# Optimization experiments

Hardware: AMD Instinct MI355X
Metric: run time of the kernel (lower is better)

The kernel has to match this reference:

```python
import jax, jax.numpy as jnp
import numpy as np

B, L, HID, D, H, HKV, EPS, THETA = 1, 2048, 2048, 128, 32, 4, 1e-6, 1000000.0
GROUPS = H // HKV  # 8


def setup_inputs() -> dict:
    key = jax.random.key(0)
    ks = jax.random.split(key, 6)
    x = jax.random.normal(ks[0], (B, L, HID), dtype=jnp.float32)
    wq = jax.random.normal(ks[1], (H * D, HID), dtype=jnp.float32) * 0.02
    wk = jax.random.normal(ks[2], (HKV * D, HID), dtype=jnp.float32) * 0.02
    wv = jax.random.normal(ks[3], (HKV * D, HID), dtype=jnp.float32) * 0.02
    wo = jax.random.normal(ks[4], (HID, H * D), dtype=jnp.float32) * 0.02
    q_norm_w = jnp.ones((D,), dtype=jnp.float32)
    k_norm_w = jnp.ones((D,), dtype=jnp.float32)
    # RoPE tables: inv_freq over half dims, emb = concat(freqs, freqs)
    inv_freq = 1.0 / (THETA ** (jnp.arange(0, D, 2, dtype=jnp.float32) / D))
    pos = jnp.arange(L, dtype=jnp.float32)
    freqs = pos[:, None] * inv_freq[None, :]        # [L, D/2]
    emb = jnp.concatenate([freqs, freqs], axis=-1)  # [L, D]
    cos = jnp.cos(emb)[None]                        # [1, L, D]
    sin = jnp.sin(emb)[None]
    return {"x": x, "wq": wq, "wk": wk, "wv": wv, "wo": wo,
            "q_norm_w": q_norm_w, "k_norm_w": k_norm_w, "cos": cos, "sin": sin}


def _rmsnorm(t, w):
    var = jnp.mean(t * t, axis=-1, keepdims=True)
    return t * jax.lax.rsqrt(var + EPS) * w


def _rotate_half(t):
    t1, t2 = jnp.split(t, 2, axis=-1)
    return jnp.concatenate([-t2, t1], axis=-1)


def reference(x, wq, wk, wv, wo, q_norm_w, k_norm_w, cos, sin):
    b, l, _ = x.shape
    # projections -> [B, heads, L, D]
    q = _rmsnorm((x @ wq.T).reshape(b, l, H, D), q_norm_w).swapaxes(1, 2)
    k = _rmsnorm((x @ wk.T).reshape(b, l, HKV, D), k_norm_w).swapaxes(1, 2)
    v = (x @ wv.T).reshape(b, l, HKV, D).swapaxes(1, 2)
    # RoPE (cos/sin broadcast over head dim)
    c, s = cos[:, None], sin[:, None]
    q = c * q + s * _rotate_half(q)
    k = c * k + s * _rotate_half(k)
    # GQA: repeat kv heads across groups
    k = jnp.repeat(k, GROUPS, axis=1)
    v = jnp.repeat(v, GROUPS, axis=1)
    # causal SDPA
    scores = jnp.einsum("bhqd,bhkd->bhqk", q, k) / np.sqrt(D).astype(np.float32)
    causal = jnp.tril(jnp.ones((l, l), dtype=bool))
    scores = jnp.where(causal, scores, jnp.finfo(scores.dtype).min)
    attn = jax.nn.softmax(scores, axis=-1)
    out = jnp.einsum("bhqk,bhkd->bhqd", attn, v)
    out = out.swapaxes(1, 2).reshape(b, l, H * D)
    return out @ wo.T
```

## Files before the change

### kernel.cpp

```cpp
#include <hip/hip_runtime.h>

typedef unsigned short u16;
typedef short bh8 __attribute__((ext_vector_type(8)));
typedef short bh4 __attribute__((ext_vector_type(4)));
typedef float f4 __attribute__((ext_vector_type(4)));
typedef u16 u16x4 __attribute__((ext_vector_type(4)));

__device__ __forceinline__ u16 f2bf(float f) {
  union { float f; unsigned u; } v; v.f = f;
  unsigned u = v.u;
  return (u16)((u + 0x7fffu + ((u >> 16) & 1u)) >> 16);
}
__device__ __forceinline__ float bf2f(u16 h) {
  union { unsigned u; float f; } v; v.u = ((unsigned)h) << 16;
  return v.f;
}
__device__ __forceinline__ float fast_exp2(float x) {
#if __has_builtin(__builtin_amdgcn_exp2f)
  return __builtin_amdgcn_exp2f(x);
#else
  float r; asm("v_exp_f32 %0, %1" : "=v"(r) : "v"(x)); return r;
#endif
}
__device__ __forceinline__ unsigned cvt_pk_bf16(float lo, float hi) {
  unsigned r;
  asm("v_cvt_pk_bf16_f32 %0, %1, %2" : "=v"(r) : "v"(lo), "v"(hi));
  return r;
}
__device__ __forceinline__ void gll16(const void* src, void* dst) {
  __builtin_amdgcn_global_load_lds((const __attribute__((address_space(1))) void*)src,
                                   (__attribute__((address_space(3))) void*)dst,
                                   16, 0, 0);
}

__global__ __launch_bounds__(256) void k_cvt_all(const float* __restrict__ x,
                                                 const float* __restrict__ wq,
                                                 const float* __restrict__ wk,
                                                 const float* __restrict__ wv,
                                                 const float* __restrict__ wo,
                                                 u16* __restrict__ dst) {
  const size_t n = 5767168;
  for (size_t idx = (size_t)blockIdx.x * 256 + threadIdx.x; idx < n; idx += 4096ull * 256) {
    const float* src; size_t off;
    if (idx < 1048576)       { src = x;  off = idx; }
    else if (idx < 3145728)  { src = wq; off = idx - 1048576; }
    else if (idx < 3407872)  { src = wk; off = idx - 3145728; }
    else if (idx < 3670016)  { src = wv; off = idx - 3407872; }
    else                     { src = wo; off = idx - 3670016; }
    f4 v = *(const f4*)(src + off * 4);
    u16x4 o;
    o.x = f2bf(v[0]); o.y = f2bf(v[1]); o.z = f2bf(v[2]); o.w = f2bf(v[3]);
    *(u16x4*)(dst + idx * 4) = o;
  }
}

template<int K, bool OUTF32, int NFR, bool FUSED>
__global__ __launch_bounds__(256) void k_gemm(const u16* __restrict__ A,
                                              const u16* __restrict__ B1,
                                              const u16* __restrict__ B2,
                                              void* __restrict__ C1,
                                              void* __restrict__ C2,
                                              u16* __restrict__ Cv,
                                              int N1, int N2, int NB1, int npx) {
  constexpr int BN = NFR * 32;
  constexpr int nk = K / 32;
  constexpr int LBB = BN / 64;
  __shared__ u16 As[3][128 * 32];
  __shared__ u16 Bs[3][BN * 32];
  const int t = threadIdx.x;
  const int lane = t & 63;
  const int w = t >> 6, wm = w >> 1, wn = w & 1;
  const int g = lane >> 4, r16 = lane & 15;
  const int bb = blockIdx.x;
  const int gl = (bb & 7) * npx + (bb >> 3);
  const int bm = gl & 15;
  int bn = gl >> 4;

  const u16* B; void* C; int N; bool vpath = false;
  if (!FUSED || bn < NB1) { B = B1; C = C1; N = N1; }
  else { bn -= NB1; B = B2; C = C2; N = N2; vpath = (bn >= 4); }
  B += (size_t)bn * BN * K;
  const u16* Ab = A + (size_t)bm * 128 * K;

  f4 acc[4][NFR] = {};

  auto STAGE = [&](int kk, int bi) {
    const int k0 = kk * 32;
#pragma unroll
    for (int i2 = 0; i2 < 2; ++i2) {
      const int s = t + 256 * i2;
      const int row = s >> 2, slot = s & 3;
      gll16(Ab + (size_t)row * K + k0 + ((slot ^ (row & 3)) * 8), As[bi] + s * 8);
    }
#pragma unroll
    for (int i2 = 0; i2 < LBB; ++i2) {
      const int s = t + 256 * i2;
      const int col = s >> 2, slot = s & 3;
      gll16(B + (size_t)col * K + k0 + ((slot ^ (col & 3)) * 8), Bs[bi] + s * 8);
    }
  };
  auto COMP = [&](int bi) {
    bh8 af[4], bfr[NFR];
    const int x4 = g ^ (r16 & 3);
#pragma unroll
    for (int m = 0; m < 4; ++m)
      af[m] = *(const bh8*)&As[bi][((wm * 64 + m * 16 + r16) * 4 + x4) * 8];
#pragma unroll
    for (int n = 0; n < NFR; ++n)
      bfr[n] = *(const bh8*)&Bs[bi][((wn * 16 * NFR + n * 16 + r16) * 4 + x4) * 8];
    __builtin_amdgcn_s_setprio(1);
#pragma unroll
    for (int m = 0; m < 4; ++m)
#pragma unroll
      for (int n = 0; n < NFR; ++n)
        acc[m][n] = __builtin_amdgcn_mfma_f32_16x16x32_bf16(af[m], bfr[n], acc[m][n], 0, 0, 0);
    __builtin_amdgcn_s_setprio(0);
  };

  STAGE(0, 0);
  STAGE(1, 1);

  int bi = 0;
  for (int k = 0; k < nk - 2; ++k) {
    int st = bi + 2; if (st >= 3) st -= 3;
    STAGE(k + 2, st);
    if constexpr (NFR == 4) asm volatile("s_waitcnt vmcnt(8)" ::: "memory");
    else                    asm volatile("s_waitcnt vmcnt(6)" ::: "memory");
    __builtin_amdgcn_s_barrier();
    __builtin_amdgcn_sched_barrier(0);
    COMP(bi);
    asm volatile("s_waitcnt lgkmcnt(0)" ::: "memory");
    __builtin_amdgcn_s_barrier();
    bi = (bi + 1 == 3) ? 0 : bi + 1;
  }
  if constexpr (NFR == 4) asm volatile("s_waitcnt vmcnt(4)" ::: "memory");
  else                    asm volatile("s_waitcnt vmcnt(3)" ::: "memory");
  __builtin_amdgcn_s_barrier();
  __builtin_amdgcn_sched_barrier(0);
  COMP(bi);
  asm volatile("s_waitcnt lgkmcnt(0)" ::: "memory");
  __builtin_amdgcn_s_barrier();
  bi = (bi + 1 == 3) ? 0 : bi + 1;
  asm volatile("s_waitcnt vmcnt(0)" ::: "memory");
  __builtin_amdgcn_s_barrier();
  __builtin_amdgcn_sched_barrier(0);
  COMP(bi);

  if constexpr (FUSED) {
    if (vpath) {
#pragma unroll
      for (int m = 0; m < 4; ++m) {
        const int lp = bm * 128 + wm * 64 + (m >> 1) * 32 + g * 8 + (m & 1) * 4;
#pragma unroll
        for (int n = 0; n < NFR; ++n) {
          const int col = bn * BN + wn * 16 * NFR + n * 16 + r16;
          union { u16x4 v; unsigned wrd[2]; } o;
          o.wrd[0] = cvt_pk_bf16(acc[m][n][0], acc[m][n][1]);
          o.wrd[1] = cvt_pk_bf16(acc[m][n][2], acc[m][n][3]);
          *(u16x4*)&Cv[(size_t)(col - 512) * 2048 + lp] = o.v;
        }
      }
      return;
    }
  }

#pragma unroll
  for (int m = 0; m < 4; ++m) {
    const int row0 = bm * 128 + wm * 64 + m * 16 + g * 4;
#pragma unroll
    for (int n = 0; n < NFR; ++n) {
      const int col = bn * BN + wn * 16 * NFR + n * 16 + r16;
#pragma unroll
      for (int r = 0; r < 4; ++r) {
        if constexpr (OUTF32)
          ((float*)C)[(size_t)(row0 + r) * N + col] = acc[m][n][r];
        else
          ((u16*)C)[(size_t)(row0 + r) * N + col] = f2bf(acc[m][n][r]);
      }
    }
  }
}

__global__ __launch_bounds__(256) void k_normrope(u16* __restrict__ qbuf,
                                                  u16* __restrict__ kvbuf,
                                                  const float* __restrict__ qw,
                                                  const float* __restrict__ kw,
                                                  const float* __restrict__ cosb,
                                                  const float* __restrict__ sinb) {
  const float CSC = 1.4426950408889634f * 0.088388347648318447f;
  const int t = threadIdx.x, lane = t & 63, w = t >> 6;
  const int rid = blockIdx.x * 4 + w;
  u16* base; const float* nw; int seq; float sc;
  if (rid < 2048 * 32) {
    seq = rid >> 5;
    base = qbuf + (size_t)seq * 4096 + (size_t)(rid & 31) * 128;
    nw = qw; sc = CSC;
  } else {
    const int r2 = rid - 2048 * 32;
    seq = r2 >> 2;
    base = kvbuf + (size_t)seq * 1024 + (size_t)(r2 & 3) * 128;
    nw = kw; sc = 1.0f;
  }
  float a = bf2f(base[lane]);
  float b = bf2f(base[lane + 64]);
  float ss = a * a + b * b;
#pragma unroll
  for (int off = 32; off >= 1; off >>= 1) ss += __shfl_xor(ss, off);
  const float rs = rsqrtf(ss * (1.0f / 128.0f) + 1e-6f);
  const float na = a * rs * nw[lane];
  const float nb = b * rs * nw[lane + 64];
  const float c1 = cosb[seq * 128 + lane],      s1 = sinb[seq * 128 + lane];
  const float c2 = cosb[seq * 128 + lane + 64], s2 = sinb[seq * 128 + lane + 64];
  base[lane]      = f2bf(sc * (c1 * na - s1 * nb));
  base[lane + 64] = f2bf(sc * (c2 * nb + s2 * na));
}

__global__ __launch_bounds__(256, 3) void k_attn(const u16* __restrict__ Q,
                                                 const u16* __restrict__ Kb,
                                                 const u16* __restrict__ Vt,
                                                 u16* __restrict__ O) {
  __shared__ u16 Ks[2][64 * 128];
  __shared__ u16 Vs[128 * 64];
  const int t = threadIdx.x, lane = t & 63, w = t >> 6;
  const int g = lane >> 4, r16 = lane & 15;
  const int b = blockIdx.x;
  const int i = b & 31;
  const int qt = 31 - (b >> 5);
  const int h = ((i >> 1) & 3) * 8 + ((i & 1) << 2) + (i >> 3);
  const int kvh = h >> 3;
  const int qw0 = qt * 64 + w * 16;
  const int qg  = qw0 + r16;

  bh8 qf[4];
#pragma unroll
  for (int kc = 0; kc < 4; ++kc)
    qf[kc] = *(const bh8*)(Q + (size_t)qg * 4096 + h * 128 + (kc * 4 + g) * 8);

  const int niter = qt + 1;

  f4 acc_o[8] = {};
  f4 acc_l = {};
  float mrun = -3.0e38f;

  bh8 ones;
#pragma unroll
  for (int z = 0; z < 8; ++z) ones[z] = (short)0x3F80;

#pragma unroll
  for (int i2 = 0; i2 < 4; ++i2) {
    const int s = t + 256 * i2, row = s >> 4, sl = s & 15;
    gll16(Kb + (size_t)row * 1024 + kvh * 128 + ((sl ^ (row & 15)) * 8), Ks[0] + s * 8);
  }
  __syncthreads();

  int cur = 0;
  for (int kt = 0; kt < niter; ++kt) {
#pragma unroll
    for (int i2 = 0; i2 < 4; ++i2) {
      const int s = t + 256 * i2, row = s >> 3, sl = s & 7;
      gll16(Vt + (size_t)(kvh * 128 + row) * 2048 + kt * 64 + ((sl ^ (row & 7)) * 8),
            Vs + s * 8);
    }
    if (kt + 1 < niter) {
      const int nt = kt + 1;
#pragma unroll
      for (int i2 = 0; i2 < 4; ++i2) {
        const int s = t + 256 * i2, row = s >> 4, sl = s & 15;
        gll16(Kb + (size_t)(nt * 64 + row) * 1024 + kvh * 128 + ((sl ^ (row & 15)) * 8),
              Ks[cur ^ 1] + s * 8);
      }
    }

    f4 st[4] = {};
    __builtin_amdgcn_s_setprio(1);
#pragma unroll
    for (int kf = 0; kf < 4; ++kf) {
      const int krow = kf * 16 + r16;
#pragma unroll
      for (int kc = 0; kc < 4; ++kc) {
        bh8 kfr = *(const bh8*)&Ks[cur][krow * 128 + (((kc * 4 + g) ^ (krow & 15)) * 8)];
        st[kf] = __builtin_amdgcn_mfma_f32_16x16x32_bf16(kfr, qf[kc], st[kf], 0, 0, 0);
      }
    }
    __builtin_amdgcn_s_setprio(0);

    if (kt == qt) {
      const int kb = kt * 64 + g * 4;
#pragma unroll
      for (int kf = 0; kf < 4; ++kf)
#pragma unroll
        for (int r = 0; r < 4; ++r)
          if (kb + kf * 16 + r > qg) st[kf][r] = -3.0e38f;
    }

    f4 m4;
#pragma unroll
    for (int r = 0; r < 4; ++r)
      m4[r] = fmaxf(fmaxf(st[0][r], st[1][r]), fmaxf(st[2][r], st[3][r]));
    float tmax = fmaxf(fmaxf(m4[0], m4[1]), fmaxf(m4[2], m4[3]));
    tmax = fmaxf(tmax, __shfl_xor(tmax, 16));
    tmax = fmaxf(tmax, __shfl_xor(tmax, 32));

    if (!__all(tmax <= mrun + 8.0f)) {
      const float mnew = fmaxf(mrun, tmax);
      const float alpha = fast_exp2(mrun - mnew);
      mrun = mnew;
      acc_l *= alpha;
#pragma unroll
      for (int d = 0; d < 8; ++d) acc_o[d] *= alpha;
    }

    union { bh8 v[2]; unsigned wrd[8]; } pu;
#pragma unroll
    for (int j = 0; j < 8; ++j) {
      const int i0 = 2 * j, i1 = 2 * j + 1;
      float p0 = fast_exp2(st[i0 >> 2][i0 & 3] - mrun);
      float p1 = fast_exp2(st[i1 >> 2][i1 & 3] - mrun);
      pu.wrd[j] = cvt_pk_bf16(p0, p1);
    }

    __syncthreads();

    __builtin_amdgcn_s_setprio(1);
#pragma unroll
    for (int c = 0; c < 2; ++c)
      acc_l = __builtin_amdgcn_mfma_f32_16x16x32_bf16(ones, pu.v[c], acc_l, 0, 0, 0);
#pragma unroll
    for (int dcol = 0; dcol < 8; ++dcol) {
      const int vrow = dcol * 16 + r16;
#pragma unroll
      for (int c = 0; c < 2; ++c) {
        const int slot = c * 4 + g;
        bh8 vfr = *(const bh8*)&Vs[vrow * 64 + ((slot ^ (vrow & 7)) * 8)];
        acc_o[dcol] = __builtin_amdgcn_mfma_f32_16x16x32_bf16(vfr, pu.v[c], acc_o[dcol], 0, 0, 0);
      }
    }
    __builtin_amdgcn_s_setprio(0);

    __syncthreads();
    cur ^= 1;
  }

  const float inv = 1.0f / acc_l[0];
#pragma unroll
  for (int dcol = 0; dcol < 8; ++dcol) {
    union { u16x4 v; unsigned wrd[2]; } o;
    o.wrd[0] = cvt_pk_bf16(acc_o[dcol][0] * inv, acc_o[dcol][1] * inv);
    o.wrd[1] = cvt_pk_bf16(acc_o[dcol][2] * inv, acc_o[dcol][3] * inv);
    *(u16x4*)&O[(size_t)qg * 4096 + h * 128 + dcol * 16 + g * 4] = o.v;
  }
}

extern "C" void kernel_launch(void* const* d_in, const int* in_sizes, int n_in,
                              void* d_out, int out_size, void* d_ws, size_t ws_size,
                              hipStream_t stream) {
  (void)in_sizes; (void)n_in; (void)out_size; (void)ws_size;
  const float* x    = (const float*)d_in[0];
  const float* wq   = (const float*)d_in[1];
  const float* wk   = (const float*)d_in[2];
  const float* wv   = (const float*)d_in[3];
  const float* wo   = (const float*)d_in[4];
  const float* qw   = (const float*)d_in[5];
  const float* kw   = (const float*)d_in[6];
  const float* cosb = (const float*)d_in[7];
  const float* sinb = (const float*)d_in[8];

  u16* xb   = (u16*)d_ws;
  u16* wqb  = xb  + (size_t)2048 * 2048;
  u16* wkvb = wqb + (size_t)4096 * 2048;
  u16* wob  = wkvb + (size_t)1024 * 2048;
  u16* qbuf = wob + (size_t)2048 * 4096;
  u16* kvb  = qbuf + (size_t)2048 * 4096;
  u16* vt   = kvb + (size_t)2048 * 1024;
  u16* aout = vt  + (size_t)512 * 2048;

  k_cvt_all<<<dim3(4096), 256, 0, stream>>>(x, wq, wk, wv, wo, xb);

  k_gemm<2048, false, 4, true><<<dim3(640), 256, 0, stream>>>(
      xb, wqb, wkvb, qbuf, kvb, vt, 4096, 1024, 32, 80);

  k_normrope<<<dim3((2048 * 36) / 4), 256, 0, stream>>>(qbuf, kvb, qw, kw, cosb, sinb);

  k_attn<<<dim3(1024), 256, 0, stream>>>(qbuf, kvb, vt, aout);

  k_gemm<4096, true, 2, false><<<dim3(512), 256, 0, stream>>>(
      aout, wob, nullptr, d_out, nullptr, nullptr, 2048, 0, 0, 64);
}
```

Before: 206.9 us.

## Deepen GEMM LDS pipeline and remap blocks to XCD-local row tiles

```diff
diff --git a/kernel.cpp b/kernel.cpp
--- a/kernel.cpp
+++ b/kernel.cpp
@@ -31,6 +31,15 @@
   __builtin_amdgcn_global_load_lds((const __attribute__((address_space(1))) void*)src,
                                    (__attribute__((address_space(3))) void*)dst,
                                    16, 0, 0);
+}
+__device__ __forceinline__ void wait_vm(int n) {
+  if (n >= 12)      asm volatile("s_waitcnt vmcnt(12)" ::: "memory");
+  else if (n == 9)  asm volatile("s_waitcnt vmcnt(9)" ::: "memory");
+  else if (n == 8)  asm volatile("s_waitcnt vmcnt(8)" ::: "memory");
+  else if (n == 6)  asm volatile("s_waitcnt vmcnt(6)" ::: "memory");
+  else if (n == 4)  asm volatile("s_waitcnt vmcnt(4)" ::: "memory");
+  else if (n == 3)  asm volatile("s_waitcnt vmcnt(3)" ::: "memory");
+  else              asm volatile("s_waitcnt vmcnt(0)" ::: "memory");
 }
 
 __global__ __launch_bounds__(256) void k_cvt_all(const float* __restrict__ x,
@@ -54,27 +63,28 @@
   }
 }
 
-template<int K, bool OUTF32, int NFR, bool FUSED>
+template<int K, bool OUTF32, int NFR, bool FUSED, int NBUF>
 __global__ __launch_bounds__(256) void k_gemm(const u16* __restrict__ A,
                                               const u16* __restrict__ B1,
                                               const u16* __restrict__ B2,
                                               void* __restrict__ C1,
                                               void* __restrict__ C2,
                                               u16* __restrict__ Cv,
-                                              int N1, int N2, int NB1, int npx) {
+                                              int N1, int N2, int NB1, int half) {
   constexpr int BN = NFR * 32;
   constexpr int nk = K / 32;
   constexpr int LBB = BN / 64;
-  __shared__ u16 As[3][128 * 32];
-  __shared__ u16 Bs[3][BN * 32];
+  constexpr int LPS = 2 + LBB;
+  __shared__ u16 As[NBUF][128 * 32];
+  __shared__ u16 Bs[NBUF][BN * 32];
   const int t = threadIdx.x;
   const int lane = t & 63;
   const int w = t >> 6, wm = w >> 1, wn = w & 1;
   const int g = lane >> 4, r16 = lane & 15;
   const int bb = blockIdx.x;
-  const int gl = (bb & 7) * npx + (bb >> 3);
-  const int bm = gl & 15;
-  int bn = gl >> 4;
+  const int xcd = bb & 7, j = bb >> 3;
+  const int bm = 2 * xcd + (j >= half ? 1 : 0);
+  int bn = (j >= half) ? (j - half) : j;
 
   const u16* B; void* C; int N; bool vpath = false;
   if (!FUSED || bn < NB1) { B = B1; C = C1; N = N1; }
@@ -117,34 +127,24 @@
     __builtin_amdgcn_s_setprio(0);
   };
 
-  STAGE(0, 0);
-  STAGE(1, 1);
+#pragma unroll
+  for (int s = 0; s < NBUF - 1; ++s) STAGE(s, s);
 
   int bi = 0;
-  for (int k = 0; k < nk - 2; ++k) {
-    int st = bi + 2; if (st >= 3) st -= 3;
-    STAGE(k + 2, st);
-    if constexpr (NFR == 4) asm volatile("s_waitcnt vmcnt(8)" ::: "memory");
-    else                    asm volatile("s_waitcnt vmcnt(6)" ::: "memory");
+  for (int k = 0; k < nk; ++k) {
+    if (k + NBUF - 1 < nk) {
+      int st = bi + NBUF - 1; if (st >= NBUF) st -= NBUF;
+      STAGE(k + NBUF - 1, st);
+    }
+    int rem = nk - 1 - k; if (rem > NBUF - 1) rem = NBUF - 1;
+    wait_vm(rem * LPS);
     __builtin_amdgcn_s_barrier();
     __builtin_amdgcn_sched_barrier(0);
     COMP(bi);
     asm volatile("s_waitcnt lgkmcnt(0)" ::: "memory");
     __builtin_amdgcn_s_barrier();
-    bi = (bi + 1 == 3) ? 0 : bi + 1;
-  }
-  if constexpr (NFR == 4) asm volatile("s_waitcnt vmcnt(4)" ::: "memory");
-  else                    asm volatile("s_waitcnt vmcnt(3)" ::: "memory");
-  __builtin_amdgcn_s_barrier();
-  __builtin_amdgcn_sched_barrier(0);
-  COMP(bi);
-  asm volatile("s_waitcnt lgkmcnt(0)" ::: "memory");
-  __builtin_amdgcn_s_barrier();
-  bi = (bi + 1 == 3) ? 0 : bi + 1;
-  asm volatile("s_waitcnt vmcnt(0)" ::: "memory");
-  __builtin_amdgcn_s_barrier();
-  __builtin_amdgcn_sched_barrier(0);
-  COMP(bi);
+    bi = (bi + 1 == NBUF) ? 0 : bi + 1;
+  }
 
   if constexpr (FUSED) {
     if (vpath) {
@@ -312,11 +312,11 @@
 
     union { bh8 v[2]; unsigned wrd[8]; } pu;
 #pragma unroll
-    for (int j = 0; j < 8; ++j) {
-      const int i0 = 2 * j, i1 = 2 * j + 1;
+    for (int j2 = 0; j2 < 8; ++j2) {
+      const int i0 = 2 * j2, i1 = 2 * j2 + 1;
       float p0 = fast_exp2(st[i0 >> 2][i0 & 3] - mrun);
       float p1 = fast_exp2(st[i1 >> 2][i1 & 3] - mrun);
-      pu.wrd[j] = cvt_pk_bf16(p0, p1);
+      pu.wrd[j2] = cvt_pk_bf16(p0, p1);
     }
 
     __syncthreads();
@@ -376,13 +376,13 @@
 
   k_cvt_all<<<dim3(4096), 256, 0, stream>>>(x, wq, wk, wv, wo, xb);
 
-  k_gemm<2048, false, 4, true><<<dim3(640), 256, 0, stream>>>(
-      xb, wqb, wkvb, qbuf, kvb, vt, 4096, 1024, 32, 80);
+  k_gemm<2048, false, 4, true, 4><<<dim3(640), 256, 0, stream>>>(
+      xb, wqb, wkvb, qbuf, kvb, vt, 4096, 1024, 32, 40);
 
   k_normrope<<<dim3((2048 * 36) / 4), 256, 0, stream>>>(qbuf, kvb, qw, kw, cosb, sinb);
 
   k_attn<<<dim3(1024), 256, 0, stream>>>(qbuf, kvb, vt, aout);
 
-  k_gemm<4096, true, 2, false><<<dim3(512), 256, 0, stream>>>(
-      aout, wob, nullptr, d_out, nullptr, nullptr, 2048, 0, 0, 64);
-}
+  k_gemm<4096, true, 2, false, 5><<<dim3(512), 256, 0, stream>>>(
+      aout, wob, nullptr, d_out, nullptr, nullptr, 2048, 0, 0, 32);
+}
```

New measurement: 248.7 us. +20.2%, slower.

## Split-K the output projection GEMM into two halves with a reduce pass

Applied to the files above, without the earlier changes.

```diff
diff --git a/kernel.cpp b/kernel.cpp
--- a/kernel.cpp
+++ b/kernel.cpp
@@ -181,6 +181,115 @@
   }
 }
 
+template<int K, int NFR>
+__global__ __launch_bounds__(256) void k_gemm_sk(const u16* __restrict__ A,
+                                                 const u16* __restrict__ Bw,
+                                                 float* __restrict__ C0,
+                                                 float* __restrict__ C1p,
+                                                 int N, int npx) {
+  constexpr int BN = NFR * 32;
+  constexpr int KLEN = K / 2;
+  constexpr int nk = KLEN / 32;
+  constexpr int LBB = BN / 64;
+  __shared__ u16 As[3][128 * 32];
+  __shared__ u16 Bs[3][BN * 32];
+  const int t = threadIdx.x;
+  const int lane = t & 63;
+  const int w = t >> 6, wm = w >> 1, wn = w & 1;
+  const int g = lane >> 4, r16 = lane & 15;
+  const int bb = blockIdx.x;
+  int gl = (bb & 7) * npx + (bb >> 3);
+  const int ks = gl >> 9; gl &= 511;
+  const int bm = gl & 15;
+  const int bn = gl >> 4;
+  float* C = ks ? C1p : C0;
+  const u16* B  = Bw + (size_t)bn * BN * K + ks * KLEN;
+  const u16* Ab = A  + (size_t)bm * 128 * K + ks * KLEN;
+
+  f4 acc[4][NFR] = {};
+
+  auto STAGE = [&](int kk, int bi) {
+    const int k0 = kk * 32;
+#pragma unroll
+    for (int i2 = 0; i2 < 2; ++i2) {
+      const int s = t + 256 * i2;
+      const int row = s >> 2, slot = s & 3;
+      gll16(Ab + (size_t)row * K + k0 + ((slot ^ (row & 3)) * 8), As[bi] + s * 8);
+    }
+#pragma unroll
+    for (int i2 = 0; i2 < LBB; ++i2) {
+      const int s = t + 256 * i2;
+      const int col = s >> 2, slot = s & 3;
+      gll16(B + (size_t)col * K + k0 + ((slot ^ (col & 3)) * 8), Bs[bi] + s * 8);
+    }
+  };
+  auto COMP = [&](int bi) {
+    bh8 af[4], bfr[NFR];
+    const int x4 = g ^ (r16 & 3);
+#pragma unroll
+    for (int m = 0; m < 4; ++m)
+      af[m] = *(const bh8*)&As[bi][((wm * 64 + m * 16 + r16) * 4 + x4) * 8];
+#pragma unroll
+    for (int n = 0; n < NFR; ++n)
+      bfr[n] = *(const bh8*)&Bs[bi][((wn * 16 * NFR + n * 16 + r16) * 4 + x4) * 8];
+    __builtin_amdgcn_s_setprio(1);
+#pragma unroll
+    for (int m = 0; m < 4; ++m)
+#pragma unroll
+      for (int n = 0; n < NFR; ++n)
+        acc[m][n] = __builtin_amdgcn_mfma_f32_16x16x32_bf16(af[m], bfr[n], acc[m][n], 0, 0, 0);
+    __builtin_amdgcn_s_setprio(0);
+  };
+
+  STAGE(0, 0);
+  STAGE(1, 1);
+
+  int bi = 0;
+  for (int k = 0; k < nk - 2; ++k) {
+    int st = bi + 2; if (st >= 3) st -= 3;
+    STAGE(k + 2, st);
+    asm volatile("s_waitcnt vmcnt(6)" ::: "memory");
+    __builtin_amdgcn_s_barrier();
+    __builtin_amdgcn_sched_barrier(0);
+    COMP(bi);
+    asm volatile("s_waitcnt lgkmcnt(0)" ::: "memory");
+    __builtin_amdgcn_s_barrier();
+    bi = (bi + 1 == 3) ? 0 : bi + 1;
+  }
+  asm volatile("s_waitcnt vmcnt(3)" ::: "memory");
+  __builtin_amdgcn_s_barrier();
+  __builtin_amdgcn_sched_barrier(0);
+  COMP(bi);
+  asm volatile("s_waitcnt lgkmcnt(0)" ::: "memory");
+  __builtin_amdgcn_s_barrier();
+  bi = (bi + 1 == 3) ? 0 : bi + 1;
+  asm volatile("s_waitcnt vmcnt(0)" ::: "memory");
+  __builtin_amdgcn_s_barrier();
+  __builtin_amdgcn_sched_barrier(0);
+  COMP(bi);
+
+#pragma unroll
+  for (int m = 0; m < 4; ++m) {
+    const int row0 = bm * 128 + wm * 64 + m * 16 + g * 4;
+#pragma unroll
+    for (int n = 0; n < NFR; ++n) {
+      const int col = bn * BN + wn * 16 * NFR + n * 16 + r16;
+#pragma unroll
+      for (int r = 0; r < 4; ++r)
+        C[(size_t)(row0 + r) * N + col] = acc[m][n][r];
+    }
+  }
+}
+
+__global__ __launch_bounds__(256) void k_reduce(float* __restrict__ out,
+                                                const float* __restrict__ part) {
+  const size_t i = (size_t)blockIdx.x * 256 + threadIdx.x;
+  f4 a = *(const f4*)(out + i * 4);
+  f4 b = *(const f4*)(part + i * 4);
+  a += b;
+  *(f4*)(out + i * 4) = a;
+}
+
 __global__ __launch_bounds__(256) void k_normrope(u16* __restrict__ qbuf,
                                                   u16* __restrict__ kvbuf,
                                                   const float* __restrict__ qw,
@@ -312,11 +421,11 @@
 
     union { bh8 v[2]; unsigned wrd[8]; } pu;
 #pragma unroll
-    for (int j = 0; j < 8; ++j) {
-      const int i0 = 2 * j, i1 = 2 * j + 1;
+    for (int j2 = 0; j2 < 8; ++j2) {
+      const int i0 = 2 * j2, i1 = 2 * j2 + 1;
       float p0 = fast_exp2(st[i0 >> 2][i0 & 3] - mrun);
       float p1 = fast_exp2(st[i1 >> 2][i1 & 3] - mrun);
-      pu.wrd[j] = cvt_pk_bf16(p0, p1);
+      pu.wrd[j2] = cvt_pk_bf16(p0, p1);
     }
 
     __syncthreads();
@@ -373,6 +482,7 @@
   u16* kvb  = qbuf + (size_t)2048 * 4096;
   u16* vt   = kvb + (size_t)2048 * 1024;
   u16* aout = vt  + (size_t)512 * 2048;
+  float* partial = (float*)wqb;
 
   k_cvt_all<<<dim3(4096), 256, 0, stream>>>(x, wq, wk, wv, wo, xb);
 
@@ -383,6 +493,8 @@
 
   k_attn<<<dim3(1024), 256, 0, stream>>>(qbuf, kvb, vt, aout);
 
-  k_gemm<4096, true, 2, false><<<dim3(512), 256, 0, stream>>>(
-      aout, wob, nullptr, d_out, nullptr, nullptr, 2048, 0, 0, 64);
-}
+  k_gemm_sk<4096, 2><<<dim3(1024), 256, 0, stream>>>(
+      aout, wob, (float*)d_out, partial, 2048, 128);
+
+  k_reduce<<<dim3(4096), 256, 0, stream>>>((float*)d_out, partial);
+}
```

Measured after the change: 200.6 us. -3.1%, faster.
